# Performance work log

Measured on AMD Instinct MI355X. Metric: run time of the kernel, lower is better.

## Reference

```python
import jax, jax.numpy as jnp
import numpy as np

EPS = 1e-05


def _rms_norm(x, w):
    xf = x.astype(jnp.float32)
    o = xf * jax.lax.rsqrt(jnp.square(xf).mean(-1, keepdims=True) + EPS)
    return (o * w.astype(jnp.float32)).astype(x.dtype)


def _apply_rope(x, sin, cos):
    # x: [B,T,N,H]; sin/cos: [B,T,H/2]
    half = x.shape[-1] // 2
    x1, x2 = x[..., :half], x[..., half:]
    s, c = sin[:, :, None, :], cos[:, :, None, :]
    return jnp.concatenate([x1 * c - x2 * s, x2 * c + x1 * s], axis=-1).astype(x.dtype)


def setup_inputs() -> dict:
    key = jax.random.key(0)
    ks = jax.random.split(key, 12)
    B, T, D, FF, HALF = 2, 1024, 4096, 12288, 64
    return {
        "x": jax.random.normal(ks[0], (B, T, D), jnp.float32),
        "sin": jax.random.uniform(ks[1], (B, T, HALF), jnp.float32),
        "cos": jax.random.uniform(ks[2], (B, T, HALF), jnp.float32),
        "attn_norm_w": jax.random.uniform(ks[3], (D,), jnp.float32),
        "ff_norm_w": jax.random.uniform(ks[4], (D,), jnp.float32),
        "wq": jax.random.normal(ks[5], (D, D), jnp.float32) * 0.02,
        "wk": jax.random.normal(ks[6], (D, D), jnp.float32) * 0.02,
        "wv": jax.random.normal(ks[7], (D, D), jnp.float32) * 0.02,
        "wo": jax.random.normal(ks[8], (D, D), jnp.float32) * 0.02,
        "w_ff": jax.random.normal(ks[9], (D, FF), jnp.float32) * 0.02,
        "w_up": jax.random.normal(ks[10], (D, FF), jnp.float32) * 0.02,
        "w_out": jax.random.normal(ks[11], (FF, D), jnp.float32) * 0.02,
    }


def reference(x, sin, cos, attn_norm_w, ff_norm_w, wq, wk, wv, wo, w_ff, w_up, w_out):
    B, T, D = x.shape
    head_dim = sin.shape[-1] * 2  # 128
    # --- attention ---
    xn = _rms_norm(x, attn_norm_w)
    q = (xn @ wq).reshape(B, T, -1, head_dim)
    k = (xn @ wk).reshape(B, T, -1, head_dim)
    v = (xn @ wv).reshape(B, T, -1, head_dim)
    q = _apply_rope(q, sin, cos)
    k = _apply_rope(k, sin, cos)
    scale = jnp.asarray(1.0 / np.sqrt(head_dim), dtype=q.dtype)
    logits = jnp.einsum("BTNH,BSNH->BNTS", q, k) * scale
    probs = jax.nn.softmax(logits.astype(jnp.float32), axis=-1).astype(k.dtype)
    attn = jnp.einsum("BNTS,BSNH->BTNH", probs, v).reshape(B, T, D)
    x = x + attn @ wo
    # --- SwiGLU MLP ---
    res = x
    xn = _rms_norm(x, ff_norm_w)
    h = jax.nn.silu(xn @ w_ff) * (xn @ w_up)
    return res + h @ w_out
```

## Files before the change

### kernel.cpp

```cpp
#include <hip/hip_runtime.h>
#include <type_traits>


#define D_MODEL 4096
#define FF_DIM  12288
#define SEQ     1024
#define NBATCH  2
#define M_ROWS  2048
#define NHEAD   32
#define HDIM    128
#define QKV_N   12288
#define FF2_N   24576

typedef short bf16x8 __attribute__((ext_vector_type(8)));
typedef ushort u16x16 __attribute__((ext_vector_type(16)));
typedef float f32x4  __attribute__((ext_vector_type(4)));

__device__ __forceinline__ ushort f2bf(float f) {
  unsigned u = __float_as_uint(f);
  u += 0x7FFFu + ((u >> 16) & 1u);
  return (ushort)(u >> 16);
}
__device__ __forceinline__ float bf2f(ushort u) {
  return __uint_as_float(((unsigned)u) << 16);
}

__device__ __forceinline__ void gload_lds16(const ushort* gsrc, ushort* ldst) {
  __builtin_amdgcn_global_load_lds((const __attribute__((address_space(1))) void*)gsrc,
                                   (__attribute__((address_space(3))) void*)ldst, 16, 0, 0);
}

#define SBAR()   asm volatile("s_barrier" ::: "memory")
#define LGKM0()  asm volatile("s_waitcnt lgkmcnt(0)" ::: "memory")
#define VMCNT8() asm volatile("s_waitcnt vmcnt(8)" ::: "memory")

__global__ __launch_bounds__(256)
void transpose_convert(const float* __restrict__ W, ushort* __restrict__ Wt,
                       int K, int N, int remap, int upoff)
{
  __shared__ float tile[64][68];
  const int t = threadIdx.x;
  const size_t k0 = (size_t)blockIdx.y * 64, n0 = (size_t)blockIdx.x * 64;
  const int lx = (t & 15) * 4, ly = t >> 4;
#pragma unroll
  for (int i = 0; i < 64; i += 16)
    *(float4*)&tile[ly + i][lx] = *(const float4*)&W[(k0 + ly + i) * N + n0 + lx];
  __syncthreads();
  const int n = t >> 2, kq = (t & 3) * 16;
  u16x16 ov;
#pragma unroll
  for (int e = 0; e < 16; e++) ov[e] = f2bf(tile[kq + e][n]);
  size_t nOut = n0 + n;
  if (remap) nOut = ((nOut >> 7) << 8) + (nOut & 127) + upoff;
  *(u16x16*)&Wt[nOut * K + k0 + kq] = ov;
}

__global__ __launch_bounds__(256)
void v_transpose(const ushort* __restrict__ v, ushort* __restrict__ vt)
{
  __shared__ ushort tile[32][33];
  const int x = threadIdx.x, y = threadIdx.y;
  const int row0 = blockIdx.x * 32;
  const int d0 = blockIdx.y * 32;
  const int h = blockIdx.z;
  const int b = row0 >> 10, sl0 = row0 & (SEQ - 1);
#pragma unroll
  for (int i = 0; i < 32; i += 8)
    tile[y + i][x] = v[(size_t)(row0 + y + i) * QKV_N + h * HDIM + d0 + x];
  __syncthreads();
  ushort* ob = vt + ((size_t)(b * NHEAD + h) * HDIM + d0) * SEQ + sl0;
#pragma unroll
  for (int i = 0; i < 32; i += 8)
    ob[(size_t)(y + i) * SEQ + x] = tile[x][y + i];
}

__global__ __launch_bounds__(256)
void rmsnorm_kernel(const float* __restrict__ x, const float* __restrict__ w,
                    ushort* __restrict__ out)
{
  const int row = blockIdx.x, t = threadIdx.x;
  const float* xr = x + (size_t)row * D_MODEL;
  float4 vv[4];
  float ss = 0.f;
#pragma unroll
  for (int p = 0; p < 4; p++) {
    vv[p] = *(const float4*)&xr[p * 1024 + t * 4];
    ss += vv[p].x * vv[p].x + vv[p].y * vv[p].y + vv[p].z * vv[p].z + vv[p].w * vv[p].w;
  }
#pragma unroll
  for (int mm = 1; mm < 64; mm <<= 1) ss += __shfl_xor(ss, mm);
  __shared__ float wsum[4];
  if ((t & 63) == 0) wsum[t >> 6] = ss;
  __syncthreads();
  ss = wsum[0] + wsum[1] + wsum[2] + wsum[3];
  const float rs = rsqrtf(ss * (1.f / 4096.f) + 1e-5f);
#pragma unroll
  for (int p = 0; p < 4; p++) {
    const float4 wv = *(const float4*)&w[p * 1024 + t * 4];
    ushort4 ov;
    ov.x = f2bf(vv[p].x * rs * wv.x);
    ov.y = f2bf(vv[p].y * rs * wv.y);
    ov.z = f2bf(vv[p].z * rs * wv.z);
    ov.w = f2bf(vv[p].w * rs * wv.w);
    *(ushort4*)&out[(size_t)row * D_MODEL + p * 1024 + t * 4] = ov;
  }
}

__global__ __launch_bounds__(256)
void rope_kernel(ushort* __restrict__ q, ushort* __restrict__ k,
                 const float* __restrict__ sinp, const float* __restrict__ cosp,
                 int ld)
{
  const size_t idx = (size_t)blockIdx.x * 256 + threadIdx.x;
  const int d = (int)(idx & 63);
  const int h = (int)((idx >> 6) & 31);
  const int t = (int)(idx >> 11);
  const float s = sinp[t * 64 + d], c = cosp[t * 64 + d];
  const size_t base = (size_t)t * ld + h * HDIM + d;
  const float q1 = bf2f(q[base]), q2 = bf2f(q[base + 64]);
  q[base]      = f2bf(q1 * c - q2 * s);
  q[base + 64] = f2bf(q2 * c + q1 * s);
  const float k1 = bf2f(k[base]), k2 = bf2f(k[base + 64]);
  k[base]      = f2bf(k1 * c - k2 * s);
  k[base + 64] = f2bf(k2 * c + k1 * s);
}

__global__ __launch_bounds__(64)
void attn_fwd(const ushort* __restrict__ q, const ushort* __restrict__ k,
              const ushort* __restrict__ vt, ushort* __restrict__ o,
              int ldq, int ldo)
{
  const int l = threadIdx.x, c16 = l & 15, g = l >> 4;
  const int qt = blockIdx.x, h = blockIdx.y, b = blockIdx.z;
  __shared__ __align__(16) ushort P_lds[2][16 * 32];

  const size_t head_off = (size_t)h * HDIM;
  const ushort* vtb = vt + (size_t)(b * NHEAD + h) * HDIM * SEQ;
  bf16x8 qf[2][4];
#pragma unroll
  for (int tile = 0; tile < 2; tile++) {
    const size_t rowQ = (size_t)(b * SEQ + qt * 32 + tile * 16 + c16);
#pragma unroll
    for (int kc = 0; kc < 4; kc++)
      qf[tile][kc] = *(const bf16x8*)(q + rowQ * ldq + head_off + kc * 32 + g * 8);
  }

  f32x4 oacc[2][8];
#pragma unroll
  for (int tile = 0; tile < 2; tile++)
#pragma unroll
    for (int i = 0; i < 8; i++) oacc[tile][i] = (f32x4){0.f, 0.f, 0.f, 0.f};
  float mrow[2][4], lsum[2][4];
#pragma unroll
  for (int tile = 0; tile < 2; tile++)
#pragma unroll
    for (int r = 0; r < 4; r++) { mrow[tile][r] = -1e30f; lsum[tile][r] = 0.f; }
  const float scale = 0.08838834764831845f;
  const float L2E = 1.4426950408889634f;

  for (int s0 = 0; s0 < SEQ; s0 += 32) {
    bf16x8 kfr[2][4];
#pragma unroll
    for (int t = 0; t < 2; t++) {
      const ushort* kb = k + (size_t)(b * SEQ + s0 + t * 16 + c16) * ldq + head_off + g * 8;
#pragma unroll
      for (int kc = 0; kc < 4; kc++) kfr[t][kc] = *(const bf16x8*)(kb + kc * 32);
    }
    f32x4 st[2][2];
#pragma unroll
    for (int tile = 0; tile < 2; tile++)
#pragma unroll
      for (int t = 0; t < 2; t++) {
        f32x4 a = (f32x4){0.f, 0.f, 0.f, 0.f};
#pragma unroll
        for (int kc = 0; kc < 4; kc++)
          a = __builtin_amdgcn_mfma_f32_16x16x32_bf16(qf[tile][kc], kfr[t][kc], a, 0, 0, 0);
        st[tile][t] = a;
      }

    float s0v[2][4], s1v[2][4];
    float worst = -1e30f;
#pragma unroll
    for (int tile = 0; tile < 2; tile++)
#pragma unroll
      for (int r = 0; r < 4; r++) {
        s0v[tile][r] = st[tile][0][r] * scale;
        s1v[tile][r] = st[tile][1][r] * scale;
        worst = fmaxf(worst, fmaxf(s0v[tile][r], s1v[tile][r]) - mrow[tile][r]);
      }

    if (__any(worst > 8.0f)) {
#pragma unroll
      for (int tile = 0; tile < 2; tile++) {
        float a4[4];
#pragma unroll
        for (int r = 0; r < 4; r++) {
          float cm = fmaxf(s0v[tile][r], s1v[tile][r]);
#pragma unroll
          for (int mm = 1; mm < 16; mm <<= 1) cm = fmaxf(cm, __shfl_xor(cm, mm));
          const float mn = fmaxf(mrow[tile][r], cm);
          a4[r] = exp2f((mrow[tile][r] - mn) * L2E);
          mrow[tile][r] = mn;
          const float p0 = exp2f((s0v[tile][r] - mn) * L2E);
          const float p1 = exp2f((s1v[tile][r] - mn) * L2E);
          lsum[tile][r] = lsum[tile][r] * a4[r] + p0 + p1;
          P_lds[tile][(g * 4 + r) * 32 + c16]      = f2bf(p0);
          P_lds[tile][(g * 4 + r) * 32 + 16 + c16] = f2bf(p1);
        }
        const f32x4 av = (f32x4){a4[0], a4[1], a4[2], a4[3]};
#pragma unroll
        for (int dbi = 0; dbi < 8; dbi++) oacc[tile][dbi] *= av;
      }
    } else {
#pragma unroll
      for (int tile = 0; tile < 2; tile++)
#pragma unroll
        for (int r = 0; r < 4; r++) {
          const float p0 = exp2f((s0v[tile][r] - mrow[tile][r]) * L2E);
          const float p1 = exp2f((s1v[tile][r] - mrow[tile][r]) * L2E);
          lsum[tile][r] += p0 + p1;
          P_lds[tile][(g * 4 + r) * 32 + c16]      = f2bf(p0);
          P_lds[tile][(g * 4 + r) * 32 + 16 + c16] = f2bf(p1);
        }
    }
    __syncthreads();
    const bf16x8 pf0 = *(const bf16x8*)&P_lds[0][c16 * 32 + g * 8];
    const bf16x8 pf1 = *(const bf16x8*)&P_lds[1][c16 * 32 + g * 8];
#pragma unroll
    for (int dbi = 0; dbi < 8; dbi++) {
      const bf16x8 vf = *(const bf16x8*)(vtb + (size_t)(dbi * 16 + c16) * SEQ + s0 + g * 8);
      oacc[0][dbi] = __builtin_amdgcn_mfma_f32_16x16x32_bf16(pf0, vf, oacc[0][dbi], 0, 0, 0);
      oacc[1][dbi] = __builtin_amdgcn_mfma_f32_16x16x32_bf16(pf1, vf, oacc[1][dbi], 0, 0, 0);
    }
    __syncthreads();
  }

#pragma unroll
  for (int tile = 0; tile < 2; tile++)
#pragma unroll
    for (int r = 0; r < 4; r++) {
#pragma unroll
      for (int mm = 1; mm < 16; mm <<= 1)
        lsum[tile][r] += __shfl_xor(lsum[tile][r], mm);
    }
#pragma unroll
  for (int tile = 0; tile < 2; tile++) {
    const size_t rowO = (size_t)(b * SEQ + qt * 32 + tile * 16 + g * 4);
#pragma unroll
    for (int dbi = 0; dbi < 8; dbi++)
#pragma unroll
      for (int r = 0; r < 4; r++)
        o[(rowO + r) * ldo + head_off + dbi * 16 + c16] =
            f2bf(oacc[tile][dbi][r] / lsum[tile][r]);
  }
}

__global__ __launch_bounds__(256)
void add3_kernel(const float* __restrict__ a, const float* __restrict__ b,
                 const float* __restrict__ c, float* __restrict__ d, int n4)
{
  for (int i = blockIdx.x * 256 + threadIdx.x; i < n4; i += gridDim.x * 256) {
    const float4 av = ((const float4*)a)[i];
    const float4 bv = ((const float4*)b)[i];
    const float4 cv = ((const float4*)c)[i];
    float4 dv;
    dv.x = av.x + bv.x + cv.x; dv.y = av.y + bv.y + cv.y;
    dv.z = av.z + bv.z + cv.z; dv.w = av.w + bv.w + cv.w;
    ((float4*)d)[i] = dv;
  }
}

template <int EPI, bool SPLITK>
__global__ __launch_bounds__(512, 2)
void gemm8p(const ushort* __restrict__ A, const ushort* __restrict__ Bt,
            const float* __restrict__ res, void* __restrict__ Cout,
            int M, int N, int Ks, int ldk)
{
  __shared__ __align__(16) ushort lds[65536];
  const int tid = threadIdx.x;
  const int w = tid >> 6, l = tid & 63;
  const int c16 = l & 15, g = l >> 4;
  const int wr = w >> 2, wc = w & 3;

  const int nwg = gridDim.x;
  const int q8 = nwg >> 3, r8 = nwg & 7;
  const int xcd = blockIdx.x & 7, loc = blockIdx.x >> 3;
  int wg = (xcd < r8 ? xcd * (q8 + 1) : r8 * (q8 + 1) + (xcd - r8) * q8) + loc;
  int kslice = 0;
  if constexpr (SPLITK) { kslice = wg >> 7; wg &= 127; }
  const size_t m0 = (size_t)(wg & 7) * 256;
  const size_t n0 = (size_t)(wg >> 3) * 256;
  const int nk = Ks >> 6;

  const int srow  = (w << 3) + (l >> 3);
  const int scolE = ((l & 7) ^ (l >> 3)) << 3;
  const ushort* gA = A  + (size_t)kslice * Ks + (m0 + srow) * (size_t)ldk + scolE;
  const ushort* gB = Bt + (size_t)kslice * Ks + (n0 + srow) * (size_t)ldk + scolE;

#define STG_A(p, h, q, tk)                                                        \
  gload_lds16(gA + (size_t)((h) * 128 + (q) * 64) * ldk + (size_t)(tk) * 64,      \
              lds + (p) * 16384 + (h) * 8192 + (q) * 4096 + (w << 9))
#define STG_B(p, h, q, tk)                                                        \
  gload_lds16(gB + (size_t)((h) * 128 + (q) * 64) * ldk + (size_t)(tk) * 64,      \
              lds + 32768 + (p) * 16384 + (h) * 8192 + (q) * 4096 + (w << 9))
#define STG_A2(p, h, tk) do { STG_A(p, h, 0, tk); STG_A(p, h, 1, tk); } while (0)
#define STG_B2(p, h, tk) do { STG_B(p, h, 0, tk); STG_B(p, h, 1, tk); } while (0)

  const int xorE = (c16 & 7) << 3;
  const int k0E = (g * 8) ^ xorE;
  const int k1E = (32 + g * 8) ^ xorE;
  const int aRow = wr * 64 + c16;
  const int bRow = wc * 32 + c16;

  const char* ldsb = (const char*)lds;
  const char* pA0 = ldsb + aRow * 128 + k0E * 2;
  const char* pA1 = ldsb + aRow * 128 + k1E * 2;
  const char* pB0 = ldsb + 65536 + bRow * 128 + k0E * 2;
  const char* pB1 = ldsb + 65536 + bRow * 128 + k1E * 2;

#define RDA(P, qm, i, kk)                                                         \
  (*(const bf16x8*)((kk ? pA1 : pA0) + (P) * 32768 + (qm) * 16384 + (i) * 2048))
#define RDB(P, qn, j, kk)                                                         \
  (*(const bf16x8*)((kk ? pB1 : pB0) + (P) * 32768 + (qn) * 16384 + (j) * 2048))

  f32x4 acc[8][4];
#pragma unroll
  for (int i = 0; i < 8; i++)
#pragma unroll
    for (int j = 0; j < 4; j++) acc[i][j] = (f32x4){0.f, 0.f, 0.f, 0.f};
  bf16x8 a[4][2], b0[2][2], b1[2][2];

  STG_A2(0, 0, 0); STG_A2(0, 1, 0); STG_B2(0, 0, 0); STG_B2(0, 1, 0);
  STG_A2(1, 0, 1); STG_A2(1, 1, 1); STG_B2(1, 0, 1); STG_B2(1, 1, 1);
  VMCNT8(); SBAR();

  auto tileBody = [&](auto Pc, int t) {
    constexpr int P = decltype(Pc)::value;
    const int tn2 = (t + 2 < nk) ? t + 2 : t + 2 - nk;

#pragma unroll
    for (int j = 0; j < 2; ++j) { b0[j][0] = RDB(P, 0, j, 0); b0[j][1] = RDB(P, 0, j, 1); }
#pragma unroll
    for (int i = 0; i < 4; ++i) { a[i][0] = RDA(P, 0, i, 0); a[i][1] = RDA(P, 0, i, 1); }
    SBAR(); LGKM0();
    __builtin_amdgcn_s_setprio(1);
#pragma unroll
    for (int i = 0; i < 4; ++i)
#pragma unroll
      for (int j = 0; j < 2; ++j)
#pragma unroll
        for (int kk = 0; kk < 2; ++kk)
          acc[i][j] = __builtin_amdgcn_mfma_f32_16x16x32_bf16(a[i][kk], b0[j][kk], acc[i][j], 0, 0, 0);
    __builtin_amdgcn_s_setprio(0);
    SBAR();

#pragma unroll
    for (int j = 0; j < 2; ++j) { b1[j][0] = RDB(P, 1, j, 0); b1[j][1] = RDB(P, 1, j, 1); }
    STG_A2(P, 0, tn2);
    STG_B2(P, 0, tn2);
    SBAR(); LGKM0();
    __builtin_amdgcn_s_setprio(1);
#pragma unroll
    for (int i = 0; i < 4; ++i)
#pragma unroll
      for (int j = 0; j < 2; ++j)
#pragma unroll
        for (int kk = 0; kk < 2; ++kk)
          acc[i][2 + j] = __builtin_amdgcn_mfma_f32_16x16x32_bf16(a[i][kk], b1[j][kk], acc[i][2 + j], 0, 0, 0);
    __builtin_amdgcn_s_setprio(0);
    SBAR();

#pragma unroll
    for (int i = 0; i < 4; ++i) { a[i][0] = RDA(P, 1, i, 0); a[i][1] = RDA(P, 1, i, 1); }
    STG_B2(P, 1, tn2);
    SBAR(); LGKM0();
    __builtin_amdgcn_s_setprio(1);
#pragma unroll
    for (int i = 0; i < 4; ++i)
#pragma unroll
      for (int j = 0; j < 2; ++j)
#pragma unroll
        for (int kk = 0; kk < 2; ++kk)
          acc[4 + i][j] = __builtin_amdgcn_mfma_f32_16x16x32_bf16(a[i][kk], b0[j][kk], acc[4 + i][j], 0, 0, 0);
    __builtin_amdgcn_s_setprio(0);
    SBAR();

    STG_A2(P, 1, tn2);
    SBAR(); LGKM0();
    __builtin_amdgcn_s_setprio(1);
#pragma unroll
    for (int i = 0; i < 4; ++i)
#pragma unroll
      for (int j = 0; j < 2; ++j)
#pragma unroll
        for (int kk = 0; kk < 2; ++kk)
          acc[4 + i][2 + j] = __builtin_amdgcn_mfma_f32_16x16x32_bf16(a[i][kk], b1[j][kk], acc[4 + i][2 + j], 0, 0, 0);
    __builtin_amdgcn_s_setprio(0);
    VMCNT8(); SBAR();
  };

  for (int t = 0; t < nk; t += 2) {
    tileBody(std::integral_constant<int, 0>{}, t);
    tileBody(std::integral_constant<int, 1>{}, t + 1);
  }

#pragma unroll
  for (int qm = 0; qm < 2; qm++)
#pragma unroll
    for (int i = 0; i < 4; i++)
#pragma unroll
      for (int qn = 0; qn < 2; qn++)
#pragma unroll
        for (int j = 0; j < 2; j++)
#pragma unroll
          for (int r = 0; r < 4; r++) {
            const size_t row = m0 + qm * 128 + wr * 64 + i * 16 + g * 4 + r;
            if constexpr (EPI == 2) {
              if (qn == 1) continue;
              const float hv = acc[qm * 4 + i][j][r];
              const float uv = acc[qm * 4 + i][2 + j][r];
              const size_t col = (n0 >> 1) + wc * 32 + j * 16 + c16;
              ((ushort*)Cout)[row * (size_t)(N >> 1) + col] =
                  f2bf((hv / (1.f + __expf(-hv))) * uv);
            } else {
              const size_t col = n0 + qn * 128 + wc * 32 + j * 16 + c16;
              const size_t idx = row * N + col;
              const float v = acc[qm * 4 + i][qn * 2 + j][r];
              if constexpr (EPI == 0)      ((ushort*)Cout)[idx] = f2bf(v);
              else if constexpr (EPI == 1) ((float*)Cout)[idx] = res[idx] + v;
              else                         ((float*)Cout)[(size_t)kslice * M * N + idx] = v;
            }
          }
#undef STG_A
#undef STG_B
#undef STG_A2
#undef STG_B2
#undef RDA
#undef RDB
}

extern "C" void kernel_launch(void* const* d_in, const int* in_sizes, int n_in,
                              void* d_out, int out_size, void* d_ws, size_t ws_size,
                              hipStream_t stream)
{
  const float* x    = (const float*)d_in[0];
  const float* sinp = (const float*)d_in[1];
  const float* cosp = (const float*)d_in[2];
  const float* anw  = (const float*)d_in[3];
  const float* fnw  = (const float*)d_in[4];
  const float* wq   = (const float*)d_in[5];
  const float* wk   = (const float*)d_in[6];
  const float* wv   = (const float*)d_in[7];
  const float* wo   = (const float*)d_in[8];
  const float* wff  = (const float*)d_in[9];
  const float* wup  = (const float*)d_in[10];
  const float* wout = (const float*)d_in[11];
  float* out = (float*)d_out;

  const size_t szDD   = (size_t)D_MODEL * D_MODEL * 2;
  const size_t szDF   = (size_t)D_MODEL * FF_DIM * 2;
  const size_t szAct2 = (size_t)M_ROWS * D_MODEL * 2;
  const size_t szAct4 = (size_t)M_ROWS * D_MODEL * 4;
  const size_t szQKV  = (size_t)M_ROWS * QKV_N * 2;
  const size_t MN     = (size_t)M_ROWS * D_MODEL;

  char* ws = (char*)d_ws;
  size_t off = 0;
  auto alloc = [&](size_t bytes) -> char* {
    char* p = ws + off;
    off += (bytes + 255) & ~(size_t)255;
    return p;
  };
  ushort* R1    = (ushort*)alloc(szDF);
  ushort* R2    = (ushort*)alloc(2 * szDF);
  ushort* wot   = (ushort*)alloc(szDD);
  ushort* xn    = (ushort*)alloc(szAct2);
  ushort* qkv   = (ushort*)alloc(szQKV);
  ushort* attnb = (ushort*)alloc(szAct2);
  float*  x2    = (float*)alloc(szAct4);
  ushort* vtb   = (ushort*)alloc(szAct2);
  float*  part  = (float*)alloc(2 * MN * 4);
  if (off > ws_size) return;

  transpose_convert<<<dim3(D_MODEL / 64, D_MODEL / 64), 256, 0, stream>>>(wq, R1, D_MODEL, D_MODEL, 0, 0);
  transpose_convert<<<dim3(D_MODEL / 64, D_MODEL / 64), 256, 0, stream>>>(wk, R1 + (size_t)D_MODEL * D_MODEL, D_MODEL, D_MODEL, 0, 0);
  transpose_convert<<<dim3(D_MODEL / 64, D_MODEL / 64), 256, 0, stream>>>(wv, R1 + 2 * (size_t)D_MODEL * D_MODEL, D_MODEL, D_MODEL, 0, 0);
  transpose_convert<<<dim3(D_MODEL / 64, D_MODEL / 64), 256, 0, stream>>>(wo, wot, D_MODEL, D_MODEL, 0, 0);
  transpose_convert<<<dim3(FF_DIM / 64, D_MODEL / 64), 256, 0, stream>>>(wff, R2, D_MODEL, FF_DIM, 1, 0);
  transpose_convert<<<dim3(FF_DIM / 64, D_MODEL / 64), 256, 0, stream>>>(wup, R2, D_MODEL, FF_DIM, 1, 128);

  rmsnorm_kernel<<<M_ROWS, 256, 0, stream>>>(x, anw, xn);
  gemm8p<0, false><<<(M_ROWS / 256) * (QKV_N / 256), 512, 0, stream>>>(xn, R1, nullptr, qkv, M_ROWS, QKV_N, D_MODEL, D_MODEL);
  transpose_convert<<<dim3(D_MODEL / 64, FF_DIM / 64), 256, 0, stream>>>(wout, R1, FF_DIM, D_MODEL, 0, 0);
  rope_kernel<<<(M_ROWS * NHEAD * 64) / 256, 256, 0, stream>>>(qkv, qkv + D_MODEL, sinp, cosp, QKV_N);
  v_transpose<<<dim3(M_ROWS / 32, HDIM / 32, NHEAD), dim3(32, 8), 0, stream>>>(qkv + 2 * D_MODEL, vtb);
  attn_fwd<<<dim3(SEQ / 32, NHEAD, NBATCH), 64, 0, stream>>>(qkv, qkv + D_MODEL, vtb, attnb, QKV_N, D_MODEL);
  gemm8p<3, true><<<256, 512, 0, stream>>>(attnb, wot, nullptr, part, M_ROWS, D_MODEL, D_MODEL / 2, D_MODEL);
  add3_kernel<<<2048, 256, 0, stream>>>(x, part, part + MN, x2, (int)(MN / 4));

  rmsnorm_kernel<<<M_ROWS, 256, 0, stream>>>(x2, fnw, xn);
  gemm8p<2, false><<<(M_ROWS / 256) * (FF2_N / 256), 512, 0, stream>>>(xn, R2, nullptr, qkv , M_ROWS, FF2_N, D_MODEL, D_MODEL);
  gemm8p<3, true><<<256, 512, 0, stream>>>(qkv, R1, nullptr, part, M_ROWS, D_MODEL, FF_DIM / 2, FF_DIM);
  add3_kernel<<<2048, 256, 0, stream>>>(x2, part, part + MN, out, (int)(MN / 4));
}
```

Baseline: 1.307 ms.

## Split-K the QKV GEMM and drop pre-MFMA barriers in gemm main loop

The QKV projection GEMM now runs as a two-way split-K launch with twice as many workgroups. It writes fp32 partials into the not-yet-used R2 buffer, and a new add2bf kernel sums them and converts to bf16. The split-K workgroup decode takes a runtime tiles-per-slice parameter, and the FF weight transposes are moved after this GEMM so R2 is free. Separately, the workgroup barrier before each LDS-wait/MFMA phase in the GEMM main loop is removed to cut synchronization stalls. The cost is extra fp32 partial traffic and a second reduction pass, and the split grid may exceed one wave of resident workgroups.

```diff
diff --git a/kernel.cpp b/kernel.cpp
--- a/kernel.cpp
+++ b/kernel.cpp
@@ -270,11 +270,29 @@
   }
 }
 
+__global__ __launch_bounds__(256)
+void add2bf_kernel(const float* __restrict__ p0, const float* __restrict__ p1,
+                   ushort* __restrict__ g, int n8)
+{
+  for (int i = blockIdx.x * 256 + threadIdx.x; i < n8; i += gridDim.x * 256) {
+    const float4 a0 = ((const float4*)p0)[i * 2];
+    const float4 a1 = ((const float4*)p0)[i * 2 + 1];
+    const float4 b0 = ((const float4*)p1)[i * 2];
+    const float4 b1 = ((const float4*)p1)[i * 2 + 1];
+    ushort ov[8];
+    ov[0] = f2bf(a0.x + b0.x); ov[1] = f2bf(a0.y + b0.y);
+    ov[2] = f2bf(a0.z + b0.z); ov[3] = f2bf(a0.w + b0.w);
+    ov[4] = f2bf(a1.x + b1.x); ov[5] = f2bf(a1.y + b1.y);
+    ov[6] = f2bf(a1.z + b1.z); ov[7] = f2bf(a1.w + b1.w);
+    *(bf16x8*)&g[(size_t)i * 8] = *(bf16x8*)ov;
+  }
+}
+
 template <int EPI, bool SPLITK>
 __global__ __launch_bounds__(512, 2)
 void gemm8p(const ushort* __restrict__ A, const ushort* __restrict__ Bt,
             const float* __restrict__ res, void* __restrict__ Cout,
-            int M, int N, int Ks, int ldk)
+            int M, int N, int Ks, int ldk, int wps)
 {
   __shared__ __align__(16) ushort lds[65536];
   const int tid = threadIdx.x;
@@ -287,7 +305,7 @@
   const int xcd = blockIdx.x & 7, loc = blockIdx.x >> 3;
   int wg = (xcd < r8 ? xcd * (q8 + 1) : r8 * (q8 + 1) + (xcd - r8) * q8) + loc;
   int kslice = 0;
-  if constexpr (SPLITK) { kslice = wg >> 7; wg &= 127; }
+  if constexpr (SPLITK) { kslice = wg / wps; wg -= kslice * wps; }
   const size_t m0 = (size_t)(wg & 7) * 256;
   const size_t n0 = (size_t)(wg >> 3) * 256;
   const int nk = Ks >> 6;
@@ -342,7 +360,7 @@
     for (int j = 0; j < 2; ++j) { b0[j][0] = RDB(P, 0, j, 0); b0[j][1] = RDB(P, 0, j, 1); }
 #pragma unroll
     for (int i = 0; i < 4; ++i) { a[i][0] = RDA(P, 0, i, 0); a[i][1] = RDA(P, 0, i, 1); }
-    SBAR(); LGKM0();
+    LGKM0();
     __builtin_amdgcn_s_setprio(1);
 #pragma unroll
     for (int i = 0; i < 4; ++i)
@@ -358,7 +376,7 @@
     for (int j = 0; j < 2; ++j) { b1[j][0] = RDB(P, 1, j, 0); b1[j][1] = RDB(P, 1, j, 1); }
     STG_A2(P, 0, tn2);
     STG_B2(P, 0, tn2);
-    SBAR(); LGKM0();
+    LGKM0();
     __builtin_amdgcn_s_setprio(1);
 #pragma unroll
     for (int i = 0; i < 4; ++i)
@@ -373,7 +391,7 @@
 #pragma unroll
     for (int i = 0; i < 4; ++i) { a[i][0] = RDA(P, 1, i, 0); a[i][1] = RDA(P, 1, i, 1); }
     STG_B2(P, 1, tn2);
-    SBAR(); LGKM0();
+    LGKM0();
     __builtin_amdgcn_s_setprio(1);
 #pragma unroll
     for (int i = 0; i < 4; ++i)
@@ -386,7 +404,7 @@
     SBAR();
 
     STG_A2(P, 1, tn2);
-    SBAR(); LGKM0();
+    LGKM0();
     __builtin_amdgcn_s_setprio(1);
 #pragma unroll
     for (int i = 0; i < 4; ++i)
@@ -463,6 +481,7 @@
   const size_t szAct4 = (size_t)M_ROWS * D_MODEL * 4;
   const size_t szQKV  = (size_t)M_ROWS * QKV_N * 2;
   const size_t MN     = (size_t)M_ROWS * D_MODEL;
+  const size_t MNq    = (size_t)M_ROWS * QKV_N;
 
   char* ws = (char*)d_ws;
   size_t off = 0;
@@ -486,20 +505,26 @@
   transpose_convert<<<dim3(D_MODEL / 64, D_MODEL / 64), 256, 0, stream>>>(wk, R1 + (size_t)D_MODEL * D_MODEL, D_MODEL, D_MODEL, 0, 0);
   transpose_convert<<<dim3(D_MODEL / 64, D_MODEL / 64), 256, 0, stream>>>(wv, R1 + 2 * (size_t)D_MODEL * D_MODEL, D_MODEL, D_MODEL, 0, 0);
   transpose_convert<<<dim3(D_MODEL / 64, D_MODEL / 64), 256, 0, stream>>>(wo, wot, D_MODEL, D_MODEL, 0, 0);
+
+  rmsnorm_kernel<<<M_ROWS, 256, 0, stream>>>(x, anw, xn);
+  float* qpart = (float*)R2;
+  gemm8p<3, true><<<2 * (M_ROWS / 256) * (QKV_N / 256), 512, 0, stream>>>(
+      xn, R1, nullptr, qpart, M_ROWS, QKV_N, D_MODEL / 2, D_MODEL,
+      (M_ROWS / 256) * (QKV_N / 256));
+  add2bf_kernel<<<2048, 256, 0, stream>>>(qpart, qpart + MNq, qkv, (int)(MNq / 8));
+
   transpose_convert<<<dim3(FF_DIM / 64, D_MODEL / 64), 256, 0, stream>>>(wff, R2, D_MODEL, FF_DIM, 1, 0);
   transpose_convert<<<dim3(FF_DIM / 64, D_MODEL / 64), 256, 0, stream>>>(wup, R2, D_MODEL, FF_DIM, 1, 128);
-
-  rmsnorm_kernel<<<M_ROWS, 256, 0, stream>>>(x, anw, xn);
-  gemm8p<0, false><<<(M_ROWS / 256) * (QKV_N / 256), 512, 0, stream>>>(xn, R1, nullptr, qkv, M_ROWS, QKV_N, D_MODEL, D_MODEL);
   transpose_convert<<<dim3(D_MODEL / 64, FF_DIM / 64), 256, 0, stream>>>(wout, R1, FF_DIM, D_MODEL, 0, 0);
+
   rope_kernel<<<(M_ROWS * NHEAD * 64) / 256, 256, 0, stream>>>(qkv, qkv + D_MODEL, sinp, cosp, QKV_N);
   v_transpose<<<dim3(M_ROWS / 32, HDIM / 32, NHEAD), dim3(32, 8), 0, stream>>>(qkv + 2 * D_MODEL, vtb);
   attn_fwd<<<dim3(SEQ / 32, NHEAD, NBATCH), 64, 0, stream>>>(qkv, qkv + D_MODEL, vtb, attnb, QKV_N, D_MODEL);
-  gemm8p<3, true><<<256, 512, 0, stream>>>(attnb, wot, nullptr, part, M_ROWS, D_MODEL, D_MODEL / 2, D_MODEL);
+  gemm8p<3, true><<<256, 512, 0, stream>>>(attnb, wot, nullptr, part, M_ROWS, D_MODEL, D_MODEL / 2, D_MODEL, 128);
   add3_kernel<<<2048, 256, 0, stream>>>(x, part, part + MN, x2, (int)(MN / 4));
 
   rmsnorm_kernel<<<M_ROWS, 256, 0, stream>>>(x2, fnw, xn);
-  gemm8p<2, false><<<(M_ROWS / 256) * (FF2_N / 256), 512, 0, stream>>>(xn, R2, nullptr, qkv , M_ROWS, FF2_N, D_MODEL, D_MODEL);
-  gemm8p<3, true><<<256, 512, 0, stream>>>(qkv, R1, nullptr, part, M_ROWS, D_MODEL, FF_DIM / 2, FF_DIM);
+  gemm8p<2, false><<<(M_ROWS / 256) * (FF2_N / 256), 512, 0, stream>>>(xn, R2, nullptr, qkv , M_ROWS, FF2_N, D_MODEL, D_MODEL, 0);
+  gemm8p<3, true><<<256, 512, 0, stream>>>(qkv, R1, nullptr, part, M_ROWS, D_MODEL, FF_DIM / 2, FF_DIM, 128);
   add3_kernel<<<2048, 256, 0, stream>>>(x2, part, part + MN, out, (int)(MN / 4));
 }
```

Result: no change. 1.317 ms (+0.7%).
